# Performance work log

Hardware: AMD Instinct MI355X
Metric: run time of the kernel (lower is better)

## Reference

```python
import jax, jax.numpy as jnp
import numpy as np

D_MODEL = 512
N_HEADS = 8
D_HEAD = 64
D_FF = 1024
EPS = 1e-5


def setup_inputs() -> dict:
    key = jax.random.key(0)
    ks = jax.random.split(key, 9)
    B, L = 4, 2048
    s = lambda fan_in: 1.0 / np.sqrt(fan_in)
    return {
        "x": jax.random.normal(ks[0], (B, L, D_MODEL), dtype=jnp.float32),
        "ln1_w": jnp.ones((D_MODEL,), jnp.float32),
        "ln1_b": jnp.zeros((D_MODEL,), jnp.float32),
        "ln2_w": jnp.ones((D_MODEL,), jnp.float32),
        "ln2_b": jnp.zeros((D_MODEL,), jnp.float32),
        "wq": jax.random.normal(ks[1], (D_MODEL, N_HEADS * D_HEAD), jnp.float32) * s(D_MODEL),
        "wk": jax.random.normal(ks[2], (D_MODEL, N_HEADS * D_HEAD), jnp.float32) * s(D_MODEL),
        "wv": jax.random.normal(ks[3], (D_MODEL, N_HEADS * D_HEAD), jnp.float32) * s(D_MODEL),
        "wo": jax.random.normal(ks[4], (N_HEADS * D_HEAD, D_MODEL), jnp.float32) * s(N_HEADS * D_HEAD),
        "w_gate": jax.random.normal(ks[5], (D_MODEL, D_FF), jnp.float32) * s(D_MODEL),
        "w_up": jax.random.normal(ks[6], (D_MODEL, D_FF), jnp.float32) * s(D_MODEL),
        "w_down": jax.random.normal(ks[7], (D_FF, D_MODEL), jnp.float32) * s(D_FF),
    }


def _layernorm(x, w, b):
    mu = jnp.mean(x, axis=-1, keepdims=True)
    var = jnp.var(x, axis=-1, keepdims=True)
    return (x - mu) * jax.lax.rsqrt(var + EPS) * w + b


def reference(x, ln1_w, ln1_b, ln2_w, ln2_b, wq, wk, wv, wo, w_gate, w_up, w_down):
    B, L, _ = x.shape
    scale = D_HEAD ** -0.5

    # --- attention sublayer (pre-LN residual) ---
    h = _layernorm(x, ln1_w, ln1_b)
    q = (h @ wq).reshape(B, L, N_HEADS, D_HEAD)  # [B,L,H,Dh]
    k = (h @ wk).reshape(B, L, N_HEADS, D_HEAD)
    v = (h @ wv).reshape(B, L, N_HEADS, D_HEAD)
    scores = jnp.einsum("bqhd,bkhd->bhqk", q, k) * scale
    # softmax computed in fp32, cast back (matches F.softmax(dtype=float32).to(q.dtype))
    attn = jax.nn.softmax(scores.astype(jnp.float32), axis=-1).astype(q.dtype)
    out = jnp.einsum("bhqk,bkhd->bqhd", attn, v).reshape(B, L, N_HEADS * D_HEAD)
    x = x + out @ wo

    # --- SwiGLU FFN sublayer (pre-LN residual) ---
    h = _layernorm(x, ln2_w, ln2_b)
    gate = jax.nn.silu(h @ w_gate)
    x = x + (gate * (h @ w_up)) @ w_down
    return x
```

## Files before the change

### kernel.cpp

```cpp
#include <hip/hip_runtime.h>
#include <hip/hip_bf16.h>
#include <math.h>

#define EPS 1e-5f

typedef __attribute__((ext_vector_type(8))) short bf16x8;
typedef __attribute__((ext_vector_type(4))) float f32x4;

#define MFMA16 __builtin_amdgcn_mfma_f32_16x16x32_bf16

__device__ __forceinline__ short f2bf(float x) {
    union { float f; unsigned u; } un; un.f = x;
    unsigned r = un.u + 0x7FFF + ((un.u >> 16) & 1);
    return (short)(r >> 16);
}
__device__ __forceinline__ float bf2f(short s) {
    union { unsigned u; float f; } un;
    un.u = ((unsigned)(unsigned short)s) << 16;
    return un.f;
}
__device__ __forceinline__ unsigned pack_bf2(float a, float b) {
    unsigned r;
    asm("v_cvt_pk_bf16_f32 %0, %1, %2" : "=v"(r) : "v"(a), "v"(b));
    return r;
}
__device__ __forceinline__ float exp2_fast(float x) {
    float r;
    asm("v_exp_f32 %0, %1" : "=v"(r) : "v"(x));
    return r;
}
__device__ __forceinline__ void load_lds16(const short* g, short* l) {
    __builtin_amdgcn_global_load_lds(
        (const __attribute__((address_space(1))) unsigned int*)g,
        (__attribute__((address_space(3))) unsigned int*)l, 16, 0, 0);
}
__device__ __forceinline__ void wait_vm0_barrier() {
    asm volatile("s_waitcnt vmcnt(0)" ::: "memory");
    __builtin_amdgcn_s_barrier();
    __builtin_amdgcn_sched_barrier(0);
}

__global__ __launch_bounds__(256) void ln_kernel_b(const float* __restrict__ in,
                                                   const float* __restrict__ w,
                                                   const float* __restrict__ bb,
                                                   short* __restrict__ out) {
    int wv = threadIdx.x >> 6, lane = threadIdx.x & 63;
    int row = blockIdx.x * 4 + wv;
    const float* x = in + (size_t)row * 512 + lane * 8;
    float4 v0 = *(const float4*)x;
    float4 v1 = *(const float4*)(x + 4);
    float s  = (v0.x + v0.y) + (v0.z + v0.w) + (v1.x + v1.y) + (v1.z + v1.w);
    float s2 = v0.x*v0.x + v0.y*v0.y + v0.z*v0.z + v0.w*v0.w
             + v1.x*v1.x + v1.y*v1.y + v1.z*v1.z + v1.w*v1.w;
#pragma unroll
    for (int off = 1; off < 64; off <<= 1) {
        s  += __shfl_xor(s, off);
        s2 += __shfl_xor(s2, off);
    }
    float mu = s * (1.f / 512.f);
    float rstd = rsqrtf(s2 * (1.f / 512.f) - mu * mu + EPS);
    const float4 wa = *(const float4*)&w[lane * 8];
    const float4 wb = *(const float4*)&w[lane * 8 + 4];
    const float4 ba = *(const float4*)&bb[lane * 8];
    const float4 bv = *(const float4*)&bb[lane * 8 + 4];
    uint4 o;
    o.x = pack_bf2((v0.x - mu) * rstd * wa.x + ba.x, (v0.y - mu) * rstd * wa.y + ba.y);
    o.y = pack_bf2((v0.z - mu) * rstd * wa.z + ba.z, (v0.w - mu) * rstd * wa.w + ba.w);
    o.z = pack_bf2((v1.x - mu) * rstd * wb.x + bv.x, (v1.y - mu) * rstd * wb.y + bv.y);
    o.w = pack_bf2((v1.z - mu) * rstd * wb.z + bv.z, (v1.w - mu) * rstd * wb.w + bv.w);
    *(uint4*)&out[(size_t)row * 512 + lane * 8] = o;
}

struct WT { const float* w; short* t; int K; int N; };
struct WT7 { WT a[7]; };
__global__ __launch_bounds__(256) void transp_w_kernel(WT7 p) {
    WT e = p.a[blockIdx.z];
    int k0 = blockIdx.x * 32, n0 = blockIdx.y * 32;
    if (k0 >= e.K || n0 >= e.N) return;
    __shared__ short t[32][33];
    int tx = threadIdx.x & 31, ty = threadIdx.x >> 5;
#pragma unroll
    for (int pp = 0; pp < 4; pp++)
        t[pp * 8 + ty][tx] = f2bf(e.w[(size_t)(k0 + pp * 8 + ty) * e.N + n0 + tx]);
    __syncthreads();
#pragma unroll
    for (int pp = 0; pp < 4; pp++)
        e.t[(size_t)(n0 + pp * 8 + ty) * e.K + k0 + tx] = t[tx][pp * 8 + ty];
}

template <int EPI>
__global__ __launch_bounds__(256) void gemm_mfma(const short* __restrict__ A,
                                                 const short* __restrict__ Bt,
                                                 const float* __restrict__ res,
                                                 const short* __restrict__ resb,
                                                 void* __restrict__ Cv,
                                                 int M, int N, int K) {
    __shared__ short As[2][128 * 64];
    __shared__ short Bs[2][128 * 64];
    const int tid = threadIdx.x;
    const int lane = tid & 63, w = tid >> 6;
    const int g = lane >> 4, r16 = lane & 15;
    const int wr = w >> 1, wc = w & 1;

    const int nb = gridDim.x * gridDim.y;
    const int fid = blockIdx.y * gridDim.x + blockIdx.x;
    const int nid = (fid & 7) * (nb >> 3) + (fid >> 3);
    const int m0 = (nid / gridDim.x) * 128, n0 = (nid % gridDim.x) * 128;

    const int lr = lane >> 3;
    const int ck = (lane & 7) ^ lr;
    const int row0 = w * 32;

    auto stage = [&](int buf, int k0) {
#pragma unroll
        for (int p = 0; p < 4; p++) {
            int rb = row0 + p * 8;
            load_lds16(&A [(size_t)(m0 + rb + lr) * K + k0 + ck * 8], &As[buf][rb * 64]);
            load_lds16(&Bt[(size_t)(n0 + rb + lr) * K + k0 + ck * 8], &Bs[buf][rb * 64]);
        }
    };

    f32x4 acc[4][4] = {};
    stage(0, 0);
    wait_vm0_barrier();

    const int nt = K >> 6;
    int cur = 0;
    for (int t = 0; t < nt; t++) {
        if (t + 1 < nt) stage(cur ^ 1, (t + 1) << 6);
#pragma unroll
        for (int ks = 0; ks < 2; ks++) {
            bf16x8 av[4], bv[4];
#pragma unroll
            for (int i = 0; i < 4; i++) {
                int row = wr * 64 + i * 16 + r16;
                av[i] = *(const bf16x8*)&As[cur][row * 64 + ((ks * 4 + g) ^ (row & 7)) * 8];
            }
#pragma unroll
            for (int j = 0; j < 4; j++) {
                int row = wc * 64 + j * 16 + r16;
                bv[j] = *(const bf16x8*)&Bs[cur][row * 64 + ((ks * 4 + g) ^ (row & 7)) * 8];
            }
#pragma unroll
            for (int i = 0; i < 4; i++)
#pragma unroll
                for (int j = 0; j < 4; j++)
                    acc[i][j] = MFMA16(av[i], bv[j], acc[i][j], 0, 0, 0);
        }
        wait_vm0_barrier();
        cur ^= 1;
    }

#pragma unroll
    for (int i = 0; i < 4; i++)
#pragma unroll
        for (int j = 0; j < 4; j++)
#pragma unroll
            for (int jr = 0; jr < 4; jr++) {
                int m = m0 + wr * 64 + i * 16 + 4 * g + jr;
                int n = n0 + wc * 64 + j * 16 + r16;
                float v = acc[i][j][jr];
                if (EPI == 0) {
                    size_t idx = (size_t)m * N + n;
                    ((float*)Cv)[idx] = res[idx] + v;
                } else if (EPI == 1) {
                    ((short*)Cv)[(size_t)m * N + n] = f2bf(v);
                } else if (EPI == 2) {
                    if (n < 512) v *= 0.18033688011112042f;
                    ((short*)Cv)[(size_t)(n >> 9) * 4194304 +
                                 (((size_t)(m >> 11) * 8 + ((n >> 6) & 7)) * 2048 + (m & 2047)) * 64 + (n & 63)] = f2bf(v);
                } else {
                    float gt = bf2f(resb[(size_t)m * N + n]);
                    float y = gt / (1.f + __expf(-gt)) * v;
                    ((short*)Cv)[(size_t)m * N + n] = f2bf(y);
                }
            }
}

__global__ __launch_bounds__(256) void transp_v_kernel(const short* __restrict__ vb,
                                                       short* __restrict__ vt) {
    __shared__ short tile[64][65];
    int l0 = blockIdx.x * 64;
    int bh = blockIdx.y;
    const size_t base = (size_t)bh * 2048 * 64;
    int tid = threadIdx.x;
#pragma unroll
    for (int p = 0; p < 4; p++) {
        int r = p * 16 + (tid >> 4);
        int c4 = (tid & 15) * 4;
        *(short4*)&tile[r][c4] = *(const short4*)&vb[base + (size_t)(l0 + r) * 64 + c4];
    }
    __syncthreads();
#pragma unroll
    for (int p = 0; p < 4; p++) {
        int d = p * 16 + (tid >> 4);
        int c4 = (tid & 15) * 4;
        short4 o;
        o.x = tile[c4 + 0][d]; o.y = tile[c4 + 1][d];
        o.z = tile[c4 + 2][d]; o.w = tile[c4 + 3][d];
        *(short4*)&vt[base + (size_t)d * 2048 + l0 + c4] = o;
    }
}

__global__ __launch_bounds__(256) void attn_mfma_kernel(const short* __restrict__ qb,
                                                        const short* __restrict__ kb,
                                                        const short* __restrict__ vt,
                                                        short* __restrict__ outb) {
    __shared__ short QP[128 * 64];
    __shared__ short Ks[2][4096];
    __shared__ short Vs[2][4096];

    const int fid = blockIdx.y * gridDim.x + blockIdx.x;
    const int nid = (fid & 7) * 64 + (fid >> 3);
    const int bh = nid >> 4, qt = nid & 15;
    const int b = bh >> 3, h = bh & 7;
    const int q0 = qt * 128;
    const size_t hb = (size_t)bh * (2048 * 64);

    const int tid = threadIdx.x;
    const int lane = tid & 63, w = tid >> 6;
    const int g = lane >> 4, r16 = lane & 15;
    const int lr = lane >> 3, ck = (lane & 7) ^ lr;
    const int rx = r16 & 7;

#pragma unroll
    for (int p = 0; p < 4; p++)
        load_lds16(&qb[hb + (size_t)(q0 + 32 * w + 8 * p + lr) * 64 + ck * 8],
                   &QP[(32 * w + 8 * p) * 64]);

    auto stageKV = [&](int buf, int kt) {
        int k0 = kt * 64;
        int rb = w * 16;
        load_lds16(&kb[hb + (size_t)(k0 + rb + lr) * 64 + ck * 8],      &Ks[buf][rb * 64]);
        load_lds16(&kb[hb + (size_t)(k0 + rb + 8 + lr) * 64 + ck * 8],  &Ks[buf][(rb + 8) * 64]);
        load_lds16(&vt[hb + (size_t)(rb + lr) * 2048 + k0 + ck * 8],     &Vs[buf][rb * 64]);
        load_lds16(&vt[hb + (size_t)(rb + 8 + lr) * 2048 + k0 + ck * 8], &Vs[buf][(rb + 8) * 64]);
    };
    stageKV(0, 0);
    wait_vm0_barrier();

    const int rowA = 32 * w + r16, rowB = rowA + 16;
    bf16x8 aqA0 = *(const bf16x8*)&QP[rowA * 64 + ((0 + g) ^ rx) * 8];
    bf16x8 aqA1 = *(const bf16x8*)&QP[rowA * 64 + ((4 + g) ^ rx) * 8];
    bf16x8 aqB0 = *(const bf16x8*)&QP[rowB * 64 + ((0 + g) ^ rx) * 8];
    bf16x8 aqB1 = *(const bf16x8*)&QP[rowB * 64 + ((4 + g) ^ rx) * 8];

    float mA = -1e30f, lA = 0.f, mB = -1e30f, lB = 0.f;
    float alA = 1.f, alB = 1.f;
    f32x4 oA[4] = {}, oB[4] = {};
    bf16x8 vf0, vf1, vf2, vf3, vf4, vf5, vf6, vf7;
    bf16x8 pfA0, pfA1, pfB0, pfB1;
    int cur = 0;

    for (int t = 0; t < 32; t++) {
        if (t + 1 < 32) stageKV(cur ^ 1, t + 1);
        const short* Kc = &Ks[cur][0];
        const short* Vc = &Vs[cur][0];

        f32x4 sA[4], sB[4];
#pragma unroll
        for (int c = 0; c < 4; c++) {
            int row = 16 * c + r16;
            bf16x8 ak0 = *(const bf16x8*)&Kc[row * 64 + ((0 + g) ^ rx) * 8];
            bf16x8 ak1 = *(const bf16x8*)&Kc[row * 64 + ((4 + g) ^ rx) * 8];
            f32x4 a1 = {}, a2 = {};
            a1 = MFMA16(ak0, aqA0, a1, 0, 0, 0);
            a1 = MFMA16(ak1, aqA1, a1, 0, 0, 0);
            a2 = MFMA16(ak0, aqB0, a2, 0, 0, 0);
            a2 = MFMA16(ak1, aqB1, a2, 0, 0, 0);
            sA[c] = a1; sB[c] = a2;
        }

        if (t > 0) {
#pragma unroll
            for (int c = 0; c < 4; c++) { oA[c] *= alA; oB[c] *= alB; }
            oA[0] = MFMA16(vf0, pfA0, oA[0], 0, 0, 0); oA[0] = MFMA16(vf1, pfA1, oA[0], 0, 0, 0);
            oB[0] = MFMA16(vf0, pfB0, oB[0], 0, 0, 0); oB[0] = MFMA16(vf1, pfB1, oB[0], 0, 0, 0);
            oA[1] = MFMA16(vf2, pfA0, oA[1], 0, 0, 0); oA[1] = MFMA16(vf3, pfA1, oA[1], 0, 0, 0);
            oB[1] = MFMA16(vf2, pfB0, oB[1], 0, 0, 0); oB[1] = MFMA16(vf3, pfB1, oB[1], 0, 0, 0);
            oA[2] = MFMA16(vf4, pfA0, oA[2], 0, 0, 0); oA[2] = MFMA16(vf5, pfA1, oA[2], 0, 0, 0);
            oB[2] = MFMA16(vf4, pfB0, oB[2], 0, 0, 0); oB[2] = MFMA16(vf5, pfB1, oB[2], 0, 0, 0);
            oA[3] = MFMA16(vf6, pfA0, oA[3], 0, 0, 0); oA[3] = MFMA16(vf7, pfA1, oA[3], 0, 0, 0);
            oB[3] = MFMA16(vf6, pfB0, oB[3], 0, 0, 0); oB[3] = MFMA16(vf7, pfB1, oB[3], 0, 0, 0);
        }

        vf0 = *(const bf16x8*)&Vc[(r16     ) * 64 + ((0 + g) ^ rx) * 8];
        vf1 = *(const bf16x8*)&Vc[(r16     ) * 64 + ((4 + g) ^ rx) * 8];
        vf2 = *(const bf16x8*)&Vc[(16 + r16) * 64 + ((0 + g) ^ rx) * 8];
        vf3 = *(const bf16x8*)&Vc[(16 + r16) * 64 + ((4 + g) ^ rx) * 8];
        vf4 = *(const bf16x8*)&Vc[(32 + r16) * 64 + ((0 + g) ^ rx) * 8];
        vf5 = *(const bf16x8*)&Vc[(32 + r16) * 64 + ((4 + g) ^ rx) * 8];
        vf6 = *(const bf16x8*)&Vc[(48 + r16) * 64 + ((0 + g) ^ rx) * 8];
        vf7 = *(const bf16x8*)&Vc[(48 + r16) * 64 + ((4 + g) ^ rx) * 8];

        float pmA = fmaxf(fmaxf(sA[0][0], sA[0][1]), fmaxf(sA[0][2], sA[0][3]));
        float pmB = fmaxf(fmaxf(sB[0][0], sB[0][1]), fmaxf(sB[0][2], sB[0][3]));
#pragma unroll
        for (int c = 1; c < 4; c++) {
            pmA = fmaxf(pmA, fmaxf(fmaxf(sA[c][0], sA[c][1]), fmaxf(sA[c][2], sA[c][3])));
            pmB = fmaxf(pmB, fmaxf(fmaxf(sB[c][0], sB[c][1]), fmaxf(sB[c][2], sB[c][3])));
        }
        pmA = fmaxf(pmA, __shfl_xor(pmA, 16)); pmA = fmaxf(pmA, __shfl_xor(pmA, 32));
        pmB = fmaxf(pmB, __shfl_xor(pmB, 16)); pmB = fmaxf(pmB, __shfl_xor(pmB, 32));
        float mnA = fmaxf(mA, pmA), mnB = fmaxf(mB, pmB);
        alA = exp2_fast(mA - mnA); alB = exp2_fast(mB - mnB);
        mA = mnA; mB = mnB;
        lA *= alA; lB *= alB;
        float rsA = 0.f, rsB = 0.f;
#pragma unroll
        for (int c = 0; c < 4; c++) {
            int colbase = 16 * c + 4 * g;
            int co = (((colbase >> 3) ^ rx) * 8) + (colbase & 7);
            {
                float p0 = exp2_fast(sA[c][0] - mA), p1 = exp2_fast(sA[c][1] - mA);
                float p2 = exp2_fast(sA[c][2] - mA), p3 = exp2_fast(sA[c][3] - mA);
                rsA += (p0 + p1) + (p2 + p3);
                unsigned long long pv = (unsigned long long)pack_bf2(p0, p1)
                                      | ((unsigned long long)pack_bf2(p2, p3) << 32);
                *(unsigned long long*)&QP[rowA * 64 + co] = pv;
            }
            {
                float p0 = exp2_fast(sB[c][0] - mB), p1 = exp2_fast(sB[c][1] - mB);
                float p2 = exp2_fast(sB[c][2] - mB), p3 = exp2_fast(sB[c][3] - mB);
                rsB += (p0 + p1) + (p2 + p3);
                unsigned long long pv = (unsigned long long)pack_bf2(p0, p1)
                                      | ((unsigned long long)pack_bf2(p2, p3) << 32);
                *(unsigned long long*)&QP[rowB * 64 + co] = pv;
            }
        }
        rsA += __shfl_xor(rsA, 16); rsA += __shfl_xor(rsA, 32); lA += rsA;
        rsB += __shfl_xor(rsB, 16); rsB += __shfl_xor(rsB, 32); lB += rsB;

        pfA0 = *(const bf16x8*)&QP[rowA * 64 + ((0 + g) ^ rx) * 8];
        pfA1 = *(const bf16x8*)&QP[rowA * 64 + ((4 + g) ^ rx) * 8];
        pfB0 = *(const bf16x8*)&QP[rowB * 64 + ((0 + g) ^ rx) * 8];
        pfB1 = *(const bf16x8*)&QP[rowB * 64 + ((4 + g) ^ rx) * 8];

        wait_vm0_barrier();
        cur ^= 1;
    }

#pragma unroll
    for (int c = 0; c < 4; c++) { oA[c] *= alA; oB[c] *= alB; }
    oA[0] = MFMA16(vf0, pfA0, oA[0], 0, 0, 0); oA[0] = MFMA16(vf1, pfA1, oA[0], 0, 0, 0);
    oB[0] = MFMA16(vf0, pfB0, oB[0], 0, 0, 0); oB[0] = MFMA16(vf1, pfB1, oB[0], 0, 0, 0);
    oA[1] = MFMA16(vf2, pfA0, oA[1], 0, 0, 0); oA[1] = MFMA16(vf3, pfA1, oA[1], 0, 0, 0);
    oB[1] = MFMA16(vf2, pfB0, oB[1], 0, 0, 0); oB[1] = MFMA16(vf3, pfB1, oB[1], 0, 0, 0);
    oA[2] = MFMA16(vf4, pfA0, oA[2], 0, 0, 0); oA[2] = MFMA16(vf5, pfA1, oA[2], 0, 0, 0);
    oB[2] = MFMA16(vf4, pfB0, oB[2], 0, 0, 0); oB[2] = MFMA16(vf5, pfB1, oB[2], 0, 0, 0);
    oA[3] = MFMA16(vf6, pfA0, oA[3], 0, 0, 0); oA[3] = MFMA16(vf7, pfA1, oA[3], 0, 0, 0);
    oB[3] = MFMA16(vf6, pfB0, oB[3], 0, 0, 0); oB[3] = MFMA16(vf7, pfB1, oB[3], 0, 0, 0);

    float ivA = 1.f / lA, ivB = 1.f / lB;
    int qa = q0 + 32 * w + r16;
#pragma unroll
    for (int c = 0; c < 4; c++) {
        int d = 16 * c + 4 * g;
        {
            unsigned long long pv = (unsigned long long)pack_bf2(oA[c][0] * ivA, oA[c][1] * ivA)
                                  | ((unsigned long long)pack_bf2(oA[c][2] * ivA, oA[c][3] * ivA) << 32);
            *(unsigned long long*)&outb[((size_t)b * 2048 + qa) * 512 + h * 64 + d] = pv;
        }
        {
            unsigned long long pv = (unsigned long long)pack_bf2(oB[c][0] * ivB, oB[c][1] * ivB)
                                  | ((unsigned long long)pack_bf2(oB[c][2] * ivB, oB[c][3] * ivB) << 32);
            *(unsigned long long*)&outb[((size_t)b * 2048 + qa + 16) * 512 + h * 64 + d] = pv;
        }
    }
}

extern "C" void kernel_launch(void* const* d_in, const int* in_sizes, int n_in,
                              void* d_out, int out_size, void* d_ws, size_t ws_size,
                              hipStream_t stream) {
    const float* x      = (const float*)d_in[0];
    const float* ln1_w  = (const float*)d_in[1];
    const float* ln1_b  = (const float*)d_in[2];
    const float* ln2_w  = (const float*)d_in[3];
    const float* ln2_b  = (const float*)d_in[4];
    const float* wq     = (const float*)d_in[5];
    const float* wk     = (const float*)d_in[6];
    const float* wv     = (const float*)d_in[7];
    const float* wo     = (const float*)d_in[8];
    const float* w_gate = (const float*)d_in[9];
    const float* w_up   = (const float*)d_in[10];
    const float* w_down = (const float*)d_in[11];
    float* out = (float*)d_out;

    const int M = 4 * 2048;
    char* ws = (char*)d_ws;
    const size_t MB = 1 << 20;
    short* h1b   = (short*)(ws);
    short* qb    = (short*)(ws + 8 * MB);
    short* kb    = (short*)(ws + 16 * MB);
    short* vb    = (short*)(ws + 24 * MB);
    short* vt    = (short*)(ws + 32 * MB);
    short* aob   = (short*)(ws + 40 * MB);
    short* g_b   = (short*)(ws + 48 * MB);
    short* u_b   = (short*)(ws + 64 * MB);
    short* qkvT  = (short*)(ws + 80 * MB);
    short* woT   = (short*)(ws + 82 * MB);
    short* wguT  = (short*)(ws + 83 * MB);
    short* wdT   = (short*)(ws + 85 * MB);
    short* h2b   = qb;

    WT7 wt;
    wt.a[0] = {wq,     qkvT,               512,  512};
    wt.a[1] = {wk,     qkvT + 512 * 512,   512,  512};
    wt.a[2] = {wv,     qkvT + 1024 * 512,  512,  512};
    wt.a[3] = {wo,     woT,                512,  512};
    wt.a[4] = {w_gate, wguT,               512, 1024};
    wt.a[5] = {w_up,   wguT + 1024 * 512,  512, 1024};
    wt.a[6] = {w_down, wdT,               1024,  512};

    transp_w_kernel<<<dim3(32, 32, 7), 256, 0, stream>>>(wt);
    ln_kernel_b<<<M / 4, 256, 0, stream>>>(x, ln1_w, ln1_b, h1b);
    gemm_mfma<2><<<dim3(12, 64), 256, 0, stream>>>(h1b, qkvT, nullptr, nullptr, qb, M, 1536, 512);
    transp_v_kernel<<<dim3(32, 32), 256, 0, stream>>>(vb, vt);
    attn_mfma_kernel<<<dim3(16, 32), 256, 0, stream>>>(qb, kb, vt, aob);
    gemm_mfma<0><<<dim3(4, 64), 256, 0, stream>>>(aob, woT, x, nullptr, out, M, 512, 512);
    ln_kernel_b<<<M / 4, 256, 0, stream>>>(out, ln2_w, ln2_b, h2b);
    gemm_mfma<1><<<dim3(8, 64), 256, 0, stream>>>(h2b, wguT, nullptr, nullptr, g_b, M, 1024, 512);
    gemm_mfma<4><<<dim3(8, 64), 256, 0, stream>>>(h2b, wguT + 1024 * 512, nullptr, g_b, u_b, M, 1024, 512);
    gemm_mfma<0><<<dim3(4, 64), 256, 0, stream>>>(u_b, wdT, out, nullptr, out, M, 512, 1024);
}
```

Baseline: 188.1 us.

## Rewrite attention with 32x32 MFMA, register-resident P via permlane swap, lazy rescale

Switches the flash-attention kernel from 16x16x32 to 32x32x16 bf16 MFMAs, computing transposed scores so each lane owns a query column. The probability matrix is converted into the next MFMA's operand in registers with v_permlane32_swap, replacing the LDS round-trip, and Q is held in registers so its LDS region is reused for V. The online-softmax rescale of the accumulators is skipped unless some row's max grows by more than 8 (log2 units), a threshold that keeps exponentials bounded. The software pipelining that overlapped the PV MFMAs of the previous tile with the current tile is removed, which may expose latency.

After: 166.4 us. 1.13x faster.

```diff
diff --git a/kernel.cpp b/kernel.cpp
--- a/kernel.cpp
+++ b/kernel.cpp
@@ -6,8 +6,10 @@
 
 typedef __attribute__((ext_vector_type(8))) short bf16x8;
 typedef __attribute__((ext_vector_type(4))) float f32x4;
+typedef __attribute__((ext_vector_type(16))) float f32x16;
 
 #define MFMA16 __builtin_amdgcn_mfma_f32_16x16x32_bf16
+#define MFMA32 __builtin_amdgcn_mfma_f32_32x32x16_bf16
 
 __device__ __forceinline__ short f2bf(float x) {
     union { float f; unsigned u; } un; un.f = x;
@@ -28,6 +30,14 @@
     float r;
     asm("v_exp_f32 %0, %1" : "=v"(r) : "v"(x));
     return r;
+}
+__device__ __forceinline__ void permswap(unsigned& a, unsigned& b) {
+    asm volatile("v_permlane32_swap_b32 %0, %1" : "+v"(a), "+v"(b));
+}
+__device__ __forceinline__ bf16x8 mk_frag(unsigned a, unsigned b, unsigned c, unsigned d) {
+    union { unsigned u[4]; bf16x8 v; } t;
+    t.u[0] = a; t.u[1] = b; t.u[2] = c; t.u[3] = d;
+    return t.v;
 }
 __device__ __forceinline__ void load_lds16(const short* g, short* l) {
     __builtin_amdgcn_global_load_lds(
@@ -206,9 +216,7 @@
                                                         const short* __restrict__ kb,
                                                         const short* __restrict__ vt,
                                                         short* __restrict__ outb) {
-    __shared__ short QP[128 * 64];
-    __shared__ short Ks[2][4096];
-    __shared__ short Vs[2][4096];
+    __shared__ short SM[16384];
 
     const int fid = blockIdx.y * gridDim.x + blockIdx.x;
     const int nid = (fid & 7) * 64 + (fid >> 3);
@@ -219,153 +227,146 @@
 
     const int tid = threadIdx.x;
     const int lane = tid & 63, w = tid >> 6;
-    const int g = lane >> 4, r16 = lane & 15;
-    const int lr = lane >> 3, ck = (lane & 7) ^ lr;
-    const int rx = r16 & 7;
+    const int hi = lane >> 5;
+    const int l31 = lane & 31;
+    const int lr = lane >> 3, ck = (lane & 7) ^ (lr & 7);
 
 #pragma unroll
     for (int p = 0; p < 4; p++)
         load_lds16(&qb[hb + (size_t)(q0 + 32 * w + 8 * p + lr) * 64 + ck * 8],
-                   &QP[(32 * w + 8 * p) * 64]);
+                   &SM[8192 + (32 * w + 8 * p) * 64]);
+    wait_vm0_barrier();
+    bf16x8 qf[4];
+    {
+        int row = 32 * w + l31;
+#pragma unroll
+        for (int ds = 0; ds < 4; ds++)
+            qf[ds] = *(const bf16x8*)&SM[8192 + row * 64 + ((2 * ds + hi) ^ (row & 7)) * 8];
+    }
+    asm volatile("s_waitcnt lgkmcnt(0)" ::: "memory");
+    __builtin_amdgcn_s_barrier();
+    __builtin_amdgcn_sched_barrier(0);
 
     auto stageKV = [&](int buf, int kt) {
         int k0 = kt * 64;
         int rb = w * 16;
-        load_lds16(&kb[hb + (size_t)(k0 + rb + lr) * 64 + ck * 8],      &Ks[buf][rb * 64]);
-        load_lds16(&kb[hb + (size_t)(k0 + rb + 8 + lr) * 64 + ck * 8],  &Ks[buf][(rb + 8) * 64]);
-        load_lds16(&vt[hb + (size_t)(rb + lr) * 2048 + k0 + ck * 8],     &Vs[buf][rb * 64]);
-        load_lds16(&vt[hb + (size_t)(rb + 8 + lr) * 2048 + k0 + ck * 8], &Vs[buf][(rb + 8) * 64]);
+        short* Kd = &SM[buf * 4096];
+        short* Vd = &SM[8192 + buf * 4096];
+        load_lds16(&kb[hb + (size_t)(k0 + rb + lr) * 64 + ck * 8],       &Kd[rb * 64]);
+        load_lds16(&kb[hb + (size_t)(k0 + rb + 8 + lr) * 64 + ck * 8],   &Kd[(rb + 8) * 64]);
+        load_lds16(&vt[hb + (size_t)(rb + lr) * 2048 + k0 + ck * 8],     &Vd[rb * 64]);
+        load_lds16(&vt[hb + (size_t)(rb + 8 + lr) * 2048 + k0 + ck * 8], &Vd[(rb + 8) * 64]);
     };
     stageKV(0, 0);
     wait_vm0_barrier();
 
-    const int rowA = 32 * w + r16, rowB = rowA + 16;
-    bf16x8 aqA0 = *(const bf16x8*)&QP[rowA * 64 + ((0 + g) ^ rx) * 8];
-    bf16x8 aqA1 = *(const bf16x8*)&QP[rowA * 64 + ((4 + g) ^ rx) * 8];
-    bf16x8 aqB0 = *(const bf16x8*)&QP[rowB * 64 + ((0 + g) ^ rx) * 8];
-    bf16x8 aqB1 = *(const bf16x8*)&QP[rowB * 64 + ((4 + g) ^ rx) * 8];
-
-    float mA = -1e30f, lA = 0.f, mB = -1e30f, lB = 0.f;
-    float alA = 1.f, alB = 1.f;
-    f32x4 oA[4] = {}, oB[4] = {};
-    bf16x8 vf0, vf1, vf2, vf3, vf4, vf5, vf6, vf7;
-    bf16x8 pfA0, pfA1, pfB0, pfB1;
+    float m_ = -1e30f, l_ = 0.f;
+    f32x16 o0 = (f32x16)(0.f), o1 = (f32x16)(0.f);
     int cur = 0;
 
     for (int t = 0; t < 32; t++) {
         if (t + 1 < 32) stageKV(cur ^ 1, t + 1);
-        const short* Kc = &Ks[cur][0];
-        const short* Vc = &Vs[cur][0];
-
-        f32x4 sA[4], sB[4];
-#pragma unroll
-        for (int c = 0; c < 4; c++) {
-            int row = 16 * c + r16;
-            bf16x8 ak0 = *(const bf16x8*)&Kc[row * 64 + ((0 + g) ^ rx) * 8];
-            bf16x8 ak1 = *(const bf16x8*)&Kc[row * 64 + ((4 + g) ^ rx) * 8];
-            f32x4 a1 = {}, a2 = {};
-            a1 = MFMA16(ak0, aqA0, a1, 0, 0, 0);
-            a1 = MFMA16(ak1, aqA1, a1, 0, 0, 0);
-            a2 = MFMA16(ak0, aqB0, a2, 0, 0, 0);
-            a2 = MFMA16(ak1, aqB1, a2, 0, 0, 0);
-            sA[c] = a1; sB[c] = a2;
-        }
-
-        if (t > 0) {
-#pragma unroll
-            for (int c = 0; c < 4; c++) { oA[c] *= alA; oB[c] *= alB; }
-            oA[0] = MFMA16(vf0, pfA0, oA[0], 0, 0, 0); oA[0] = MFMA16(vf1, pfA1, oA[0], 0, 0, 0);
-            oB[0] = MFMA16(vf0, pfB0, oB[0], 0, 0, 0); oB[0] = MFMA16(vf1, pfB1, oB[0], 0, 0, 0);
-            oA[1] = MFMA16(vf2, pfA0, oA[1], 0, 0, 0); oA[1] = MFMA16(vf3, pfA1, oA[1], 0, 0, 0);
-            oB[1] = MFMA16(vf2, pfB0, oB[1], 0, 0, 0); oB[1] = MFMA16(vf3, pfB1, oB[1], 0, 0, 0);
-            oA[2] = MFMA16(vf4, pfA0, oA[2], 0, 0, 0); oA[2] = MFMA16(vf5, pfA1, oA[2], 0, 0, 0);
-            oB[2] = MFMA16(vf4, pfB0, oB[2], 0, 0, 0); oB[2] = MFMA16(vf5, pfB1, oB[2], 0, 0, 0);
-            oA[3] = MFMA16(vf6, pfA0, oA[3], 0, 0, 0); oA[3] = MFMA16(vf7, pfA1, oA[3], 0, 0, 0);
-            oB[3] = MFMA16(vf6, pfB0, oB[3], 0, 0, 0); oB[3] = MFMA16(vf7, pfB1, oB[3], 0, 0, 0);
-        }
-
-        vf0 = *(const bf16x8*)&Vc[(r16     ) * 64 + ((0 + g) ^ rx) * 8];
-        vf1 = *(const bf16x8*)&Vc[(r16     ) * 64 + ((4 + g) ^ rx) * 8];
-        vf2 = *(const bf16x8*)&Vc[(16 + r16) * 64 + ((0 + g) ^ rx) * 8];
-        vf3 = *(const bf16x8*)&Vc[(16 + r16) * 64 + ((4 + g) ^ rx) * 8];
-        vf4 = *(const bf16x8*)&Vc[(32 + r16) * 64 + ((0 + g) ^ rx) * 8];
-        vf5 = *(const bf16x8*)&Vc[(32 + r16) * 64 + ((4 + g) ^ rx) * 8];
-        vf6 = *(const bf16x8*)&Vc[(48 + r16) * 64 + ((0 + g) ^ rx) * 8];
-        vf7 = *(const bf16x8*)&Vc[(48 + r16) * 64 + ((4 + g) ^ rx) * 8];
-
-        float pmA = fmaxf(fmaxf(sA[0][0], sA[0][1]), fmaxf(sA[0][2], sA[0][3]));
-        float pmB = fmaxf(fmaxf(sB[0][0], sB[0][1]), fmaxf(sB[0][2], sB[0][3]));
-#pragma unroll
-        for (int c = 1; c < 4; c++) {
-            pmA = fmaxf(pmA, fmaxf(fmaxf(sA[c][0], sA[c][1]), fmaxf(sA[c][2], sA[c][3])));
-            pmB = fmaxf(pmB, fmaxf(fmaxf(sB[c][0], sB[c][1]), fmaxf(sB[c][2], sB[c][3])));
-        }
-        pmA = fmaxf(pmA, __shfl_xor(pmA, 16)); pmA = fmaxf(pmA, __shfl_xor(pmA, 32));
-        pmB = fmaxf(pmB, __shfl_xor(pmB, 16)); pmB = fmaxf(pmB, __shfl_xor(pmB, 32));
-        float mnA = fmaxf(mA, pmA), mnB = fmaxf(mB, pmB);
-        alA = exp2_fast(mA - mnA); alB = exp2_fast(mB - mnB);
-        mA = mnA; mB = mnB;
-        lA *= alA; lB *= alB;
-        float rsA = 0.f, rsB = 0.f;
-#pragma unroll
-        for (int c = 0; c < 4; c++) {
-            int colbase = 16 * c + 4 * g;
-            int co = (((colbase >> 3) ^ rx) * 8) + (colbase & 7);
-            {
-                float p0 = exp2_fast(sA[c][0] - mA), p1 = exp2_fast(sA[c][1] - mA);
-                float p2 = exp2_fast(sA[c][2] - mA), p3 = exp2_fast(sA[c][3] - mA);
-                rsA += (p0 + p1) + (p2 + p3);
-                unsigned long long pv = (unsigned long long)pack_bf2(p0, p1)
-                                      | ((unsigned long long)pack_bf2(p2, p3) << 32);
-                *(unsigned long long*)&QP[rowA * 64 + co] = pv;
+        const short* Kc = &SM[cur * 4096];
+        const short* Vc = &SM[8192 + cur * 4096];
+
+        f32x16 s0 = (f32x16)(0.f), s1 = (f32x16)(0.f);
+        {
+            int r0 = l31, r1 = 32 + l31;
+            int cshift = (l31 & 7);
+#pragma unroll
+            for (int ds = 0; ds < 4; ds++) {
+                bf16x8 k0f = *(const bf16x8*)&Kc[r0 * 64 + ((2 * ds + hi) ^ cshift) * 8];
+                bf16x8 k1f = *(const bf16x8*)&Kc[r1 * 64 + ((2 * ds + hi) ^ cshift) * 8];
+                s0 = MFMA32(k0f, qf[ds], s0, 0, 0, 0);
+                s1 = MFMA32(k1f, qf[ds], s1, 0, 0, 0);
             }
-            {
-                float p0 = exp2_fast(sB[c][0] - mB), p1 = exp2_fast(sB[c][1] - mB);
-                float p2 = exp2_fast(sB[c][2] - mB), p3 = exp2_fast(sB[c][3] - mB);
-                rsB += (p0 + p1) + (p2 + p3);
-                unsigned long long pv = (unsigned long long)pack_bf2(p0, p1)
-                                      | ((unsigned long long)pack_bf2(p2, p3) << 32);
-                *(unsigned long long*)&QP[rowB * 64 + co] = pv;
+        }
+
+        float q0m = fmaxf(fmaxf(s0[0], s0[1]),  fmaxf(s0[2], s0[3]));
+        float q1m = fmaxf(fmaxf(s0[4], s0[5]),  fmaxf(s0[6], s0[7]));
+        float q2m = fmaxf(fmaxf(s0[8], s0[9]),  fmaxf(s0[10], s0[11]));
+        float q3m = fmaxf(fmaxf(s0[12], s0[13]), fmaxf(s0[14], s0[15]));
+        float q4m = fmaxf(fmaxf(s1[0], s1[1]),  fmaxf(s1[2], s1[3]));
+        float q5m = fmaxf(fmaxf(s1[4], s1[5]),  fmaxf(s1[6], s1[7]));
+        float q6m = fmaxf(fmaxf(s1[8], s1[9]),  fmaxf(s1[10], s1[11]));
+        float q7m = fmaxf(fmaxf(s1[12], s1[13]), fmaxf(s1[14], s1[15]));
+        float om = fmaxf(fmaxf(fmaxf(q0m, q1m), fmaxf(q2m, q3m)),
+                         fmaxf(fmaxf(q4m, q5m), fmaxf(q6m, q7m)));
+        unsigned ua = __float_as_uint(om), ub = ua;
+        permswap(ua, ub);
+        float pm = fmaxf(__uint_as_float(ua), __uint_as_float(ub));
+
+        if (!__all(pm - m_ <= 8.f)) {
+            float mn = fmaxf(m_, pm);
+            float al = exp2_fast(m_ - mn);
+            l_ *= al;
+            o0 *= al;
+            o1 *= al;
+            m_ = mn;
+        }
+
+        float rs = 0.f;
+#pragma unroll
+        for (int r = 0; r < 16; r++) { s0[r] = exp2_fast(s0[r] - m_); rs += s0[r]; }
+#pragma unroll
+        for (int r = 0; r < 16; r++) { s1[r] = exp2_fast(s1[r] - m_); rs += s1[r]; }
+        l_ += rs;
+
+        bf16x8 pf[4];
+#pragma unroll
+        for (int ks = 0; ks < 2; ks++) {
+            unsigned X0 = pack_bf2(s0[8 * ks + 0], s0[8 * ks + 1]);
+            unsigned X1 = pack_bf2(s0[8 * ks + 2], s0[8 * ks + 3]);
+            unsigned Y0 = pack_bf2(s0[8 * ks + 4], s0[8 * ks + 5]);
+            unsigned Y1 = pack_bf2(s0[8 * ks + 6], s0[8 * ks + 7]);
+            permswap(X0, Y0);
+            permswap(X1, Y1);
+            pf[ks] = mk_frag(X0, X1, Y0, Y1);
+        }
+#pragma unroll
+        for (int ks = 0; ks < 2; ks++) {
+            unsigned X0 = pack_bf2(s1[8 * ks + 0], s1[8 * ks + 1]);
+            unsigned X1 = pack_bf2(s1[8 * ks + 2], s1[8 * ks + 3]);
+            unsigned Y0 = pack_bf2(s1[8 * ks + 4], s1[8 * ks + 5]);
+            unsigned Y1 = pack_bf2(s1[8 * ks + 6], s1[8 * ks + 7]);
+            permswap(X0, Y0);
+            permswap(X1, Y1);
+            pf[2 + ks] = mk_frag(X0, X1, Y0, Y1);
+        }
+
+        {
+            int r0 = l31, r1 = 32 + l31;
+            int cs0 = r0 & 7, cs1 = r1 & 7;
+#pragma unroll
+            for (int kk = 0; kk < 4; kk++) {
+                int kc = 2 * kk + hi;
+                bf16x8 v0f = *(const bf16x8*)&Vc[r0 * 64 + (kc ^ cs0) * 8];
+                bf16x8 v1f = *(const bf16x8*)&Vc[r1 * 64 + (kc ^ cs1) * 8];
+                o0 = MFMA32(v0f, pf[kk], o0, 0, 0, 0);
+                o1 = MFMA32(v1f, pf[kk], o1, 0, 0, 0);
             }
         }
-        rsA += __shfl_xor(rsA, 16); rsA += __shfl_xor(rsA, 32); lA += rsA;
-        rsB += __shfl_xor(rsB, 16); rsB += __shfl_xor(rsB, 32); lB += rsB;
-
-        pfA0 = *(const bf16x8*)&QP[rowA * 64 + ((0 + g) ^ rx) * 8];
-        pfA1 = *(const bf16x8*)&QP[rowA * 64 + ((4 + g) ^ rx) * 8];
-        pfB0 = *(const bf16x8*)&QP[rowB * 64 + ((0 + g) ^ rx) * 8];
-        pfB1 = *(const bf16x8*)&QP[rowB * 64 + ((4 + g) ^ rx) * 8];
 
         wait_vm0_barrier();
         cur ^= 1;
     }
 
-#pragma unroll
-    for (int c = 0; c < 4; c++) { oA[c] *= alA; oB[c] *= alB; }
-    oA[0] = MFMA16(vf0, pfA0, oA[0], 0, 0, 0); oA[0] = MFMA16(vf1, pfA1, oA[0], 0, 0, 0);
-    oB[0] = MFMA16(vf0, pfB0, oB[0], 0, 0, 0); oB[0] = MFMA16(vf1, pfB1, oB[0], 0, 0, 0);
-    oA[1] = MFMA16(vf2, pfA0, oA[1], 0, 0, 0); oA[1] = MFMA16(vf3, pfA1, oA[1], 0, 0, 0);
-    oB[1] = MFMA16(vf2, pfB0, oB[1], 0, 0, 0); oB[1] = MFMA16(vf3, pfB1, oB[1], 0, 0, 0);
-    oA[2] = MFMA16(vf4, pfA0, oA[2], 0, 0, 0); oA[2] = MFMA16(vf5, pfA1, oA[2], 0, 0, 0);
-    oB[2] = MFMA16(vf4, pfB0, oB[2], 0, 0, 0); oB[2] = MFMA16(vf5, pfB1, oB[2], 0, 0, 0);
-    oA[3] = MFMA16(vf6, pfA0, oA[3], 0, 0, 0); oA[3] = MFMA16(vf7, pfA1, oA[3], 0, 0, 0);
-    oB[3] = MFMA16(vf6, pfB0, oB[3], 0, 0, 0); oB[3] = MFMA16(vf7, pfB1, oB[3], 0, 0, 0);
-
-    float ivA = 1.f / lA, ivB = 1.f / lB;
-    int qa = q0 + 32 * w + r16;
-#pragma unroll
-    for (int c = 0; c < 4; c++) {
-        int d = 16 * c + 4 * g;
-        {
-            unsigned long long pv = (unsigned long long)pack_bf2(oA[c][0] * ivA, oA[c][1] * ivA)
-                                  | ((unsigned long long)pack_bf2(oA[c][2] * ivA, oA[c][3] * ivA) << 32);
-            *(unsigned long long*)&outb[((size_t)b * 2048 + qa) * 512 + h * 64 + d] = pv;
-        }
-        {
-            unsigned long long pv = (unsigned long long)pack_bf2(oB[c][0] * ivB, oB[c][1] * ivB)
-                                  | ((unsigned long long)pack_bf2(oB[c][2] * ivB, oB[c][3] * ivB) << 32);
-            *(unsigned long long*)&outb[((size_t)b * 2048 + qa + 16) * 512 + h * 64 + d] = pv;
-        }
+    unsigned sa = __float_as_uint(l_), sb = sa;
+    permswap(sa, sb);
+    float inv = 1.f / (__uint_as_float(sa) + __uint_as_float(sb));
+    int q = q0 + 32 * w + l31;
+    size_t obase = ((size_t)b * 2048 + q) * 512 + h * 64;
+#pragma unroll
+    for (int rr = 0; rr < 4; rr++) {
+        int d0 = 8 * rr + 4 * hi;
+        unsigned long long pv =
+            (unsigned long long)pack_bf2(o0[4 * rr + 0] * inv, o0[4 * rr + 1] * inv)
+          | ((unsigned long long)pack_bf2(o0[4 * rr + 2] * inv, o0[4 * rr + 3] * inv) << 32);
+        *(unsigned long long*)&outb[obase + d0] = pv;
+        unsigned long long pv2 =
+            (unsigned long long)pack_bf2(o1[4 * rr + 0] * inv, o1[4 * rr + 1] * inv)
+          | ((unsigned long long)pack_bf2(o1[4 * rr + 2] * inv, o1[4 * rr + 3] * inv) << 32);
+        *(unsigned long long*)&outb[obase + 32 + d0] = pv2;
     }
 }
 
```
